# Kernel tuning notes

Hardware: AMD Instinct MI355X
Metric: run time of the kernel (lower is better)

The kernel has to match this reference:

```python
import jax, jax.numpy as jnp
import numpy as np

N = 50000
E = 600000
H = 128


def setup_inputs() -> dict:
    key = jax.random.key(0)
    ks = jax.random.split(key, 9)
    x = jax.random.normal(ks[0], (N, H), dtype=jnp.float32)
    edge_index = jax.random.randint(ks[1], (2, E), 0, N, dtype=jnp.int64)
    edge_weight = jax.random.uniform(ks[2], (E,), dtype=jnp.float32)
    s = 1.0 / np.sqrt(H)
    Wq = jax.random.normal(ks[3], (H, H), dtype=jnp.float32) * s
    bq = jnp.zeros((H,), dtype=jnp.float32)
    Wk = jax.random.normal(ks[4], (H, H), dtype=jnp.float32) * s
    bk = jnp.zeros((H,), dtype=jnp.float32)
    Wv = jax.random.normal(ks[5], (H, H), dtype=jnp.float32) * s
    bv = jnp.zeros((H,), dtype=jnp.float32)
    return {"x": x, "edge_index": edge_index, "edge_weight": edge_weight,
            "Wq": Wq, "bq": bq, "Wk": Wk, "bk": bk, "Wv": Wv, "bv": bv}


def reference(x, edge_index, edge_weight, Wq, bq, Wk, bk, Wv, bv):
    scale = jnp.sqrt(jnp.asarray(x.shape[-1], dtype=x.dtype))
    Q = x @ Wq.T + bq  # [N, H]
    K = x @ Wk.T + bk
    V = x @ Wv.T + bv
    row, col = edge_index[0], edge_index[1]  # [E]
    # per-edge scaled dot-product
    energy = jnp.sum(Q[row] * K[col], axis=-1) / scale  # [E]
    # NOTE: faithful to the source — softmax over ALL edges (dim=0), not per-node
    attn = jax.nn.softmax(energy * edge_weight, axis=0)  # [E]
    msgs = V[col] * attn[:, None]  # [E, H]
    out = jnp.zeros_like(x).at[row].add(msgs)  # scatter-add to destination nodes
    return out
```

## Files before the change

### kernel.cpp

```cpp
#include <hip/hip_runtime.h>
#include <hip/hip_bf16.h>

#define N_NODES 50000
#define E_EDGES 600000
#define HDIM    128

#define QKV_BLOCKS  ((N_NODES + 63) / 64)
#define EDGE_BLOCKS ((E_EDGES + 255) / 256)
#define SCAN_BLOCKS ((N_NODES + 255) / 256)
#define ROW_BLOCKS  (N_NODES / 4)

typedef float f32x4  __attribute__((ext_vector_type(4)));
typedef short short8 __attribute__((ext_vector_type(8)));

__device__ __forceinline__ unsigned short f2bf(float f) {
    __hip_bfloat16 h = __float2bfloat16(f);
    return *reinterpret_cast<unsigned short*>(&h);
}

__global__ __launch_bounds__(256) void qkv_mfma_kernel(
    const float* __restrict__ x,
    const float* __restrict__ Wq, const float* __restrict__ bq,
    const float* __restrict__ Wk, const float* __restrict__ bk,
    const float* __restrict__ Wv, const float* __restrict__ bv,
    float* __restrict__ Q, unsigned short* __restrict__ Kb,
    unsigned short* __restrict__ Vb)
{
    __shared__ __align__(16) unsigned short Ah[64 * HDIM];
    __shared__ __align__(16) unsigned short Al[64 * HDIM];
    const int r0  = blockIdx.x * 64;
    const int mat = blockIdx.y;

    for (int t = threadIdx.x; t < 2048; t += 256) {
        const int r  = t >> 5;
        const int k4 = t & 31;
        int gr = r0 + r; if (gr >= N_NODES) gr = N_NODES - 1;
        const float4 xv = *(const float4*)&x[(size_t)gr * HDIM + k4 * 4];
        const unsigned ux = __float_as_uint(xv.x), uy = __float_as_uint(xv.y);
        const unsigned uz = __float_as_uint(xv.z), uw = __float_as_uint(xv.w);
        ushort4 hv, lv;
        hv.x = (unsigned short)(ux >> 16); hv.y = (unsigned short)(uy >> 16);
        hv.z = (unsigned short)(uz >> 16); hv.w = (unsigned short)(uw >> 16);
        lv.x = f2bf(xv.x - __uint_as_float(ux & 0xffff0000u));
        lv.y = f2bf(xv.y - __uint_as_float(uy & 0xffff0000u));
        lv.z = f2bf(xv.z - __uint_as_float(uz & 0xffff0000u));
        lv.w = f2bf(xv.w - __uint_as_float(uw & 0xffff0000u));
        const int byte = (r << 8) + (k4 << 3);
        const int swz  = byte ^ ((r & 7) << 4);
        *(ushort4*)((char*)Ah + swz) = hv;
        *(ushort4*)((char*)Al + swz) = lv;
    }

    const int lane = threadIdx.x & 63;
    const int w    = threadIdx.x >> 6;
    const int lrow = lane & 15;
    const int lgrp = lane >> 4;
    const int nb   = w * 32;

    const float* Wm = (mat == 0) ? Wq : (mat == 1) ? Wk : Wv;
    const float* bm = (mat == 0) ? bq : (mat == 1) ? bk : bv;

    short8 Bh[2][4], Bl[2][4];
#pragma unroll
    for (int st = 0; st < 2; ++st) {
        const int col = nb + st * 16 + lrow;
#pragma unroll
        for (int ks = 0; ks < 4; ++ks) {
            const int k0 = ks * 32 + lgrp * 8;
            const float* p = Wm + (size_t)col * HDIM + k0;
            const float4 a = *(const float4*)p;
            const float4 b = *(const float4*)(p + 4);
            const float f[8] = {a.x, a.y, a.z, a.w, b.x, b.y, b.z, b.w};
            short8 h, l;
#pragma unroll
            for (int j = 0; j < 8; ++j) {
                const unsigned u = __float_as_uint(f[j]);
                h[j] = (short)(u >> 16);
                l[j] = (short)f2bf(f[j] - __uint_as_float(u & 0xffff0000u));
            }
            Bh[st][ks] = h; Bl[st][ks] = l;
        }
    }
    const float bias0 = bm[nb + lrow];
    const float bias1 = bm[nb + 16 + lrow];

    __syncthreads();

#pragma unroll
    for (int s = 0; s < 4; ++s) {
        f32x4 acc0 = {0.f, 0.f, 0.f, 0.f};
        f32x4 acc1 = {0.f, 0.f, 0.f, 0.f};
        const int row = s * 16 + lrow;
#pragma unroll
        for (int ks = 0; ks < 4; ++ks) {
            const int byte = (row << 8) + ((ks * 32 + lgrp * 8) << 1);
            const int swz  = byte ^ ((row & 7) << 4);
            const short8 ah = *(const short8*)((const char*)Ah + swz);
            const short8 al = *(const short8*)((const char*)Al + swz);
            acc0 = __builtin_amdgcn_mfma_f32_16x16x32_bf16(ah, Bh[0][ks], acc0, 0, 0, 0);
            acc0 = __builtin_amdgcn_mfma_f32_16x16x32_bf16(al, Bh[0][ks], acc0, 0, 0, 0);
            acc0 = __builtin_amdgcn_mfma_f32_16x16x32_bf16(ah, Bl[0][ks], acc0, 0, 0, 0);
            acc1 = __builtin_amdgcn_mfma_f32_16x16x32_bf16(ah, Bh[1][ks], acc1, 0, 0, 0);
            acc1 = __builtin_amdgcn_mfma_f32_16x16x32_bf16(al, Bh[1][ks], acc1, 0, 0, 0);
            acc1 = __builtin_amdgcn_mfma_f32_16x16x32_bf16(ah, Bl[1][ks], acc1, 0, 0, 0);
        }
        const int orow0 = r0 + s * 16 + lgrp * 4;
        if (mat == 0) {
#pragma unroll
            for (int i = 0; i < 4; ++i) {
                const int row_o = orow0 + i;
                if (row_o < N_NODES) {
                    Q[(size_t)row_o * HDIM + nb + lrow]      = acc0[i] + bias0;
                    Q[(size_t)row_o * HDIM + nb + 16 + lrow] = acc1[i] + bias1;
                }
            }
        } else {
            unsigned short* dst = (mat == 1) ? Kb : Vb;
#pragma unroll
            for (int i = 0; i < 4; ++i) {
                const int row_o = orow0 + i;
                if (row_o < N_NODES) {
                    dst[(size_t)row_o * HDIM + nb + lrow]      = f2bf(acc0[i] + bias0);
                    dst[(size_t)row_o * HDIM + nb + 16 + lrow] = f2bf(acc1[i] + bias1);
                }
            }
        }
    }
}

__global__ __launch_bounds__(256) void hist_kernel(
    const int* __restrict__ ei, int* __restrict__ counts)
{
    const int e = blockIdx.x * 256 + threadIdx.x;
    if (e < E_EDGES) atomicAdd(&counts[ei[e]], 1);
}

__global__ __launch_bounds__(256) void scan_partial_kernel(
    const int* __restrict__ counts, int* __restrict__ offs, int* __restrict__ aux)
{
    __shared__ int s[256];
    const int i = blockIdx.x * 256 + threadIdx.x;
    const int v = (i < N_NODES) ? counts[i] : 0;
    s[threadIdx.x] = v;
    __syncthreads();
    for (int d = 1; d < 256; d <<= 1) {
        int t = (threadIdx.x >= d) ? s[threadIdx.x - d] : 0;
        __syncthreads();
        s[threadIdx.x] += t;
        __syncthreads();
    }
    if (i < N_NODES) offs[i] = s[threadIdx.x] - v;
    if (threadIdx.x == 255) aux[blockIdx.x] = s[255];
}

__global__ __launch_bounds__(256) void scan_aux_kernel(int* __restrict__ aux)
{
    __shared__ int s[256];
    const int i = threadIdx.x;
    const int v = (i < SCAN_BLOCKS) ? aux[i] : 0;
    s[i] = v;
    __syncthreads();
    for (int d = 1; d < 256; d <<= 1) {
        int t = (i >= d) ? s[i - d] : 0;
        __syncthreads();
        s[i] += t;
        __syncthreads();
    }
    if (i < SCAN_BLOCKS) aux[i] = s[i] - v;
}

__global__ __launch_bounds__(256) void scan_add_kernel(
    int* __restrict__ offs, const int* __restrict__ aux, int* __restrict__ cursor)
{
    const int i = blockIdx.x * 256 + threadIdx.x;
    if (i < N_NODES) {
        const int o = offs[i] + aux[blockIdx.x];
        offs[i] = o;
        cursor[i] = o;
    }
}

__global__ __launch_bounds__(256) void bin_kernel(
    const int* __restrict__ ei, const float* __restrict__ ew,
    int* __restrict__ cursor, uint2* __restrict__ erec)
{
    const int e = blockIdx.x * 256 + threadIdx.x;
    if (e >= E_EDGES) return;
    const int row = ei[e];
    const int pos = atomicAdd(&cursor[row], 1);
    erec[pos] = make_uint2((unsigned)ei[E_EDGES + e], __float_as_uint(ew[e]));
}

__global__ __launch_bounds__(256) void energy_kernel(
    const float* __restrict__ Q, const unsigned short* __restrict__ Kb,
    const int* __restrict__ offs, const int* __restrict__ counts,
    uint2* __restrict__ erec, float* __restrict__ blockmax)
{
    const int row  = (blockIdx.x * 256 + threadIdx.x) >> 6;
    const int lane = threadIdx.x & 63;
    const int eg   = lane >> 4;
    const int sl   = lane & 15;
    const int start = offs[row], len = counts[row];
    const float4 q0 = *(const float4*)&Q[(size_t)row * HDIM + sl * 8];
    const float4 q1 = *(const float4*)&Q[(size_t)row * HDIM + sl * 8 + 4];
    const uint4* kb128 = (const uint4*)Kb;
    const float inv_scale = 0.08838834764831845f;
    float lmax = -3.4e38f;
    for (int j0 = 0; j0 < len; j0 += 8) {
        const int  jA = j0 + eg,      jB = j0 + 4 + eg;
        const bool vA = jA < len,     vB = jB < len;
        const int  eA = start + (vA ? jA : 0);
        const int  eB = start + (vB ? jB : 0);
        const uint2 rA = erec[eA];
        const uint2 rB = erec[eB];
        const uint4 uA = kb128[(size_t)rA.x * 16 + sl];
        const uint4 uB = kb128[(size_t)rB.x * 16 + sl];
        float dA = q0.x * __uint_as_float(uA.x << 16)
                 + q0.y * __uint_as_float(uA.x & 0xffff0000u)
                 + q0.z * __uint_as_float(uA.y << 16)
                 + q0.w * __uint_as_float(uA.y & 0xffff0000u)
                 + q1.x * __uint_as_float(uA.z << 16)
                 + q1.y * __uint_as_float(uA.z & 0xffff0000u)
                 + q1.z * __uint_as_float(uA.w << 16)
                 + q1.w * __uint_as_float(uA.w & 0xffff0000u);
        float dB = q0.x * __uint_as_float(uB.x << 16)
                 + q0.y * __uint_as_float(uB.x & 0xffff0000u)
                 + q0.z * __uint_as_float(uB.y << 16)
                 + q0.w * __uint_as_float(uB.y & 0xffff0000u)
                 + q1.x * __uint_as_float(uB.z << 16)
                 + q1.y * __uint_as_float(uB.z & 0xffff0000u)
                 + q1.z * __uint_as_float(uB.w << 16)
                 + q1.w * __uint_as_float(uB.w & 0xffff0000u);
#pragma unroll
        for (int m = 8; m >= 1; m >>= 1) {
            dA += __shfl_xor(dA, m);
            dB += __shfl_xor(dB, m);
        }
        const float enA = dA * inv_scale * __uint_as_float(rA.y);
        const float enB = dB * inv_scale * __uint_as_float(rB.y);
        if (vA) {
            lmax = fmaxf(lmax, enA);
            if (sl == 0) ((float*)erec)[2 * eA + 1] = enA;
        }
        if (vB) {
            lmax = fmaxf(lmax, enB);
            if (sl == 0) ((float*)erec)[2 * eB + 1] = enB;
        }
    }
#pragma unroll
    for (int m = 32; m >= 1; m >>= 1) lmax = fmaxf(lmax, __shfl_xor(lmax, m));
    __shared__ float sm[4];
    if (lane == 0) sm[threadIdx.x >> 6] = lmax;
    __syncthreads();
    if (threadIdx.x == 0)
        blockmax[blockIdx.x] = fmaxf(fmaxf(sm[0], sm[1]), fmaxf(sm[2], sm[3]));
}

__global__ __launch_bounds__(256) void reduce_max_kernel(
    const float* __restrict__ bm, int n, float* __restrict__ gmax)
{
    float m = -3.4e38f;
    for (int i = threadIdx.x; i < n; i += 256) m = fmaxf(m, bm[i]);
#pragma unroll
    for (int s = 32; s >= 1; s >>= 1) m = fmaxf(m, __shfl_xor(m, s));
    __shared__ float sm[4];
    if ((threadIdx.x & 63) == 0) sm[threadIdx.x >> 6] = m;
    __syncthreads();
    if (threadIdx.x == 0) *gmax = fmaxf(fmaxf(sm[0], sm[1]), fmaxf(sm[2], sm[3]));
}

__global__ __launch_bounds__(256) void expsum_kernel(
    uint2* __restrict__ erec, const float* __restrict__ gmax,
    float* __restrict__ blocksum)
{
    const float m = *gmax;
    const int e = blockIdx.x * 256 + threadIdx.x;
    float p = 0.f;
    if (e < E_EDGES) {
        const uint2 r = erec[e];
        p = __expf(__uint_as_float(r.y) - m);
        erec[e] = make_uint2(r.x, __float_as_uint(p));
    }
#pragma unroll
    for (int s = 32; s >= 1; s >>= 1) p += __shfl_xor(p, s);
    __shared__ float sm[4];
    if ((threadIdx.x & 63) == 0) sm[threadIdx.x >> 6] = p;
    __syncthreads();
    if (threadIdx.x == 0) blocksum[blockIdx.x] = sm[0] + sm[1] + sm[2] + sm[3];
}

__global__ __launch_bounds__(256) void reduce_sum_kernel(
    const float* __restrict__ bs, int n, float* __restrict__ gsum)
{
    float v = 0.f;
    for (int i = threadIdx.x; i < n; i += 256) v += bs[i];
#pragma unroll
    for (int s = 32; s >= 1; s >>= 1) v += __shfl_xor(v, s);
    __shared__ float sm[4];
    if ((threadIdx.x & 63) == 0) sm[threadIdx.x >> 6] = v;
    __syncthreads();
    if (threadIdx.x == 0) *gsum = sm[0] + sm[1] + sm[2] + sm[3];
}

__global__ __launch_bounds__(256) void accum_kernel(
    const unsigned short* __restrict__ Vb,
    const int* __restrict__ offs, const int* __restrict__ counts,
    const uint2* __restrict__ erec, const float* __restrict__ gsum,
    float* __restrict__ out)
{
    const int row  = (blockIdx.x * 256 + threadIdx.x) >> 6;
    const int lane = threadIdx.x & 63;
    const int eg   = lane >> 4;
    const int sl   = lane & 15;
    const float inv = 1.0f / *gsum;
    const int start = offs[row], len = counts[row];
    const uint4* vb128 = (const uint4*)Vb;
    float aA[8] = {0.f, 0.f, 0.f, 0.f, 0.f, 0.f, 0.f, 0.f};
    float aB[8] = {0.f, 0.f, 0.f, 0.f, 0.f, 0.f, 0.f, 0.f};
    for (int j0 = 0; j0 < len; j0 += 8) {
        const int  jA = j0 + eg,      jB = j0 + 4 + eg;
        const bool vA = jA < len,     vB = jB < len;
        const int  eA = start + (vA ? jA : 0);
        const int  eB = start + (vB ? jB : 0);
        const uint2 rA = erec[eA];
        const uint2 rB = erec[eB];
        const float wA = vA ? __uint_as_float(rA.y) * inv : 0.f;
        const float wB = vB ? __uint_as_float(rB.y) * inv : 0.f;
        const uint4 uA = vb128[(size_t)rA.x * 16 + sl];
        const uint4 uB = vb128[(size_t)rB.x * 16 + sl];
        aA[0] += __uint_as_float(uA.x << 16) * wA;
        aA[1] += __uint_as_float(uA.x & 0xffff0000u) * wA;
        aA[2] += __uint_as_float(uA.y << 16) * wA;
        aA[3] += __uint_as_float(uA.y & 0xffff0000u) * wA;
        aA[4] += __uint_as_float(uA.z << 16) * wA;
        aA[5] += __uint_as_float(uA.z & 0xffff0000u) * wA;
        aA[6] += __uint_as_float(uA.w << 16) * wA;
        aA[7] += __uint_as_float(uA.w & 0xffff0000u) * wA;
        aB[0] += __uint_as_float(uB.x << 16) * wB;
        aB[1] += __uint_as_float(uB.x & 0xffff0000u) * wB;
        aB[2] += __uint_as_float(uB.y << 16) * wB;
        aB[3] += __uint_as_float(uB.y & 0xffff0000u) * wB;
        aB[4] += __uint_as_float(uB.z << 16) * wB;
        aB[5] += __uint_as_float(uB.z & 0xffff0000u) * wB;
        aB[6] += __uint_as_float(uB.w << 16) * wB;
        aB[7] += __uint_as_float(uB.w & 0xffff0000u) * wB;
    }
    float a[8];
#pragma unroll
    for (int i = 0; i < 8; ++i) {
        a[i] = aA[i] + aB[i];
        a[i] += __shfl_xor(a[i], 16);
        a[i] += __shfl_xor(a[i], 32);
    }
    if (eg == 0) {
        float* o = out + (size_t)row * HDIM + sl * 8;
        *(float4*)o       = make_float4(a[0], a[1], a[2], a[3]);
        *(float4*)(o + 4) = make_float4(a[4], a[5], a[6], a[7]);
    }
}

extern "C" void kernel_launch(void* const* d_in, const int* in_sizes, int n_in,
                              void* d_out, int out_size, void* d_ws, size_t ws_size,
                              hipStream_t stream)
{
    const float* x  = (const float*)d_in[0];
    const int*   ei = (const int*)d_in[1];
    const float* ew = (const float*)d_in[2];
    const float* Wq = (const float*)d_in[3];
    const float* bq = (const float*)d_in[4];
    const float* Wk = (const float*)d_in[5];
    const float* bk = (const float*)d_in[6];
    const float* Wv = (const float*)d_in[7];
    const float* bv = (const float*)d_in[8];
    float* out = (float*)d_out;

    float* ws = (float*)d_ws;
    float* Q       = ws;
    unsigned short* Kb = (unsigned short*)(Q + (size_t)N_NODES * HDIM);
    unsigned short* Vb = Kb + (size_t)N_NODES * HDIM;
    int*   counts  = (int*)(Vb + (size_t)N_NODES * HDIM);
    int*   offs    = counts + N_NODES;
    int*   cursor  = offs + N_NODES;
    int*   aux     = cursor + N_NODES;
    uint2* erec    = (uint2*)(aux + 256);
    float* blockmax= (float*)(erec + E_EDGES);
    float* blocksum= blockmax + ROW_BLOCKS;
    float* gmax    = blocksum + EDGE_BLOCKS;
    float* gsum    = gmax + 1;

    hipMemsetAsync(counts, 0, N_NODES * sizeof(int), stream);

    qkv_mfma_kernel<<<dim3(QKV_BLOCKS, 3), 256, 0, stream>>>(
        x, Wq, bq, Wk, bk, Wv, bv, Q, Kb, Vb);
    hist_kernel<<<EDGE_BLOCKS, 256, 0, stream>>>(ei, counts);
    scan_partial_kernel<<<SCAN_BLOCKS, 256, 0, stream>>>(counts, offs, aux);
    scan_aux_kernel<<<1, 256, 0, stream>>>(aux);
    scan_add_kernel<<<SCAN_BLOCKS, 256, 0, stream>>>(offs, aux, cursor);
    bin_kernel<<<EDGE_BLOCKS, 256, 0, stream>>>(ei, ew, cursor, erec);
    energy_kernel<<<ROW_BLOCKS, 256, 0, stream>>>(Q, Kb, offs, counts, erec, blockmax);
    reduce_max_kernel<<<1, 256, 0, stream>>>(blockmax, ROW_BLOCKS, gmax);
    expsum_kernel<<<EDGE_BLOCKS, 256, 0, stream>>>(erec, gmax, blocksum);
    reduce_sum_kernel<<<1, 256, 0, stream>>>(blocksum, EDGE_BLOCKS, gsum);
    accum_kernel<<<ROW_BLOCKS, 256, 0, stream>>>(Vb, offs, counts, erec, gsum, out);
}
```

Before: 188.5 us.

## Replace single-block reductions with global atomics and merge QKV projections per block

Removes the two single-block reduce kernels for the softmax max and sum. They are replaced by an atomicMax on an order-preserving unsigned encoding of the float, and by a float atomicAdd issued from each block. The QKV projection kernel now loops over the three weight matrices inside one block, so the x tile staged in shared memory is reused instead of being reloaded by three separate blocks. This trades kernel launches and x reloads for atomic contention and lower grid parallelism in the QKV kernel, and float atomicAdd makes the sum order nondeterministic.

```diff
diff --git a/kernel.cpp b/kernel.cpp
--- a/kernel.cpp
+++ b/kernel.cpp
@@ -16,6 +16,15 @@
 __device__ __forceinline__ unsigned short f2bf(float f) {
     __hip_bfloat16 h = __float2bfloat16(f);
     return *reinterpret_cast<unsigned short*>(&h);
+}
+
+__device__ __forceinline__ unsigned fenc(float f) {
+    unsigned u = __float_as_uint(f);
+    return (u & 0x80000000u) ? ~u : (u | 0x80000000u);
+}
+__device__ __forceinline__ float fdec(unsigned v) {
+    unsigned u = (v & 0x80000000u) ? (v ^ 0x80000000u) : ~v;
+    return __uint_as_float(u);
 }
 
 __global__ __launch_bounds__(256) void qkv_mfma_kernel(
@@ -28,8 +37,7 @@
 {
     __shared__ __align__(16) unsigned short Ah[64 * HDIM];
     __shared__ __align__(16) unsigned short Al[64 * HDIM];
-    const int r0  = blockIdx.x * 64;
-    const int mat = blockIdx.y;
+    const int r0 = blockIdx.x * 64;
 
     for (int t = threadIdx.x; t < 2048; t += 256) {
         const int r  = t >> 5;
@@ -50,6 +58,7 @@
         *(ushort4*)((char*)Ah + swz) = hv;
         *(ushort4*)((char*)Al + swz) = lv;
     }
+    __syncthreads();
 
     const int lane = threadIdx.x & 63;
     const int w    = threadIdx.x >> 6;
@@ -57,71 +66,71 @@
     const int lgrp = lane >> 4;
     const int nb   = w * 32;
 
-    const float* Wm = (mat == 0) ? Wq : (mat == 1) ? Wk : Wv;
-    const float* bm = (mat == 0) ? bq : (mat == 1) ? bk : bv;
-
-    short8 Bh[2][4], Bl[2][4];
-#pragma unroll
-    for (int st = 0; st < 2; ++st) {
-        const int col = nb + st * 16 + lrow;
-#pragma unroll
-        for (int ks = 0; ks < 4; ++ks) {
-            const int k0 = ks * 32 + lgrp * 8;
-            const float* p = Wm + (size_t)col * HDIM + k0;
-            const float4 a = *(const float4*)p;
-            const float4 b = *(const float4*)(p + 4);
-            const float f[8] = {a.x, a.y, a.z, a.w, b.x, b.y, b.z, b.w};
-            short8 h, l;
-#pragma unroll
-            for (int j = 0; j < 8; ++j) {
-                const unsigned u = __float_as_uint(f[j]);
-                h[j] = (short)(u >> 16);
-                l[j] = (short)f2bf(f[j] - __uint_as_float(u & 0xffff0000u));
+    for (int mat = 0; mat < 3; ++mat) {
+        const float* Wm = (mat == 0) ? Wq : (mat == 1) ? Wk : Wv;
+        const float* bm = (mat == 0) ? bq : (mat == 1) ? bk : bv;
+
+        short8 Bh[2][4], Bl[2][4];
+#pragma unroll
+        for (int st = 0; st < 2; ++st) {
+            const int col = nb + st * 16 + lrow;
+#pragma unroll
+            for (int ks = 0; ks < 4; ++ks) {
+                const int k0 = ks * 32 + lgrp * 8;
+                const float* p = Wm + (size_t)col * HDIM + k0;
+                const float4 a = *(const float4*)p;
+                const float4 b = *(const float4*)(p + 4);
+                const float f[8] = {a.x, a.y, a.z, a.w, b.x, b.y, b.z, b.w};
+                short8 h, l;
+#pragma unroll
+                for (int j = 0; j < 8; ++j) {
+                    const unsigned u = __float_as_uint(f[j]);
+                    h[j] = (short)(u >> 16);
+                    l[j] = (short)f2bf(f[j] - __uint_as_float(u & 0xffff0000u));
+                }
+                Bh[st][ks] = h; Bl[st][ks] = l;
             }
-            Bh[st][ks] = h; Bl[st][ks] = l;
-        }
-    }
-    const float bias0 = bm[nb + lrow];
-    const float bias1 = bm[nb + 16 + lrow];
-
-    __syncthreads();
-
-#pragma unroll
-    for (int s = 0; s < 4; ++s) {
-        f32x4 acc0 = {0.f, 0.f, 0.f, 0.f};
-        f32x4 acc1 = {0.f, 0.f, 0.f, 0.f};
-        const int row = s * 16 + lrow;
-#pragma unroll
-        for (int ks = 0; ks < 4; ++ks) {
-            const int byte = (row << 8) + ((ks * 32 + lgrp * 8) << 1);
-            const int swz  = byte ^ ((row & 7) << 4);
-            const short8 ah = *(const short8*)((const char*)Ah + swz);
-            const short8 al = *(const short8*)((const char*)Al + swz);
-            acc0 = __builtin_amdgcn_mfma_f32_16x16x32_bf16(ah, Bh[0][ks], acc0, 0, 0, 0);
-            acc0 = __builtin_amdgcn_mfma_f32_16x16x32_bf16(al, Bh[0][ks], acc0, 0, 0, 0);
-            acc0 = __builtin_amdgcn_mfma_f32_16x16x32_bf16(ah, Bl[0][ks], acc0, 0, 0, 0);
-            acc1 = __builtin_amdgcn_mfma_f32_16x16x32_bf16(ah, Bh[1][ks], acc1, 0, 0, 0);
-            acc1 = __builtin_amdgcn_mfma_f32_16x16x32_bf16(al, Bh[1][ks], acc1, 0, 0, 0);
-            acc1 = __builtin_amdgcn_mfma_f32_16x16x32_bf16(ah, Bl[1][ks], acc1, 0, 0, 0);
-        }
-        const int orow0 = r0 + s * 16 + lgrp * 4;
-        if (mat == 0) {
-#pragma unroll
-            for (int i = 0; i < 4; ++i) {
-                const int row_o = orow0 + i;
-                if (row_o < N_NODES) {
-                    Q[(size_t)row_o * HDIM + nb + lrow]      = acc0[i] + bias0;
-                    Q[(size_t)row_o * HDIM + nb + 16 + lrow] = acc1[i] + bias1;
+        }
+        const float bias0 = bm[nb + lrow];
+        const float bias1 = bm[nb + 16 + lrow];
+
+#pragma unroll
+        for (int s = 0; s < 4; ++s) {
+            f32x4 acc0 = {0.f, 0.f, 0.f, 0.f};
+            f32x4 acc1 = {0.f, 0.f, 0.f, 0.f};
+            const int row = s * 16 + lrow;
+#pragma unroll
+            for (int ks = 0; ks < 4; ++ks) {
+                const int byte = (row << 8) + ((ks * 32 + lgrp * 8) << 1);
+                const int swz  = byte ^ ((row & 7) << 4);
+                const short8 ah = *(const short8*)((const char*)Ah + swz);
+                const short8 al = *(const short8*)((const char*)Al + swz);
+                acc0 = __builtin_amdgcn_mfma_f32_16x16x32_bf16(ah, Bh[0][ks], acc0, 0, 0, 0);
+                acc0 = __builtin_amdgcn_mfma_f32_16x16x32_bf16(al, Bh[0][ks], acc0, 0, 0, 0);
+                acc0 = __builtin_amdgcn_mfma_f32_16x16x32_bf16(ah, Bl[0][ks], acc0, 0, 0, 0);
+                acc1 = __builtin_amdgcn_mfma_f32_16x16x32_bf16(ah, Bh[1][ks], acc1, 0, 0, 0);
+                acc1 = __builtin_amdgcn_mfma_f32_16x16x32_bf16(al, Bh[1][ks], acc1, 0, 0, 0);
+                acc1 = __builtin_amdgcn_mfma_f32_16x16x32_bf16(ah, Bl[1][ks], acc1, 0, 0, 0);
+            }
+            const int orow0 = r0 + s * 16 + lgrp * 4;
+            if (mat == 0) {
+#pragma unroll
+                for (int i = 0; i < 4; ++i) {
+                    const int row_o = orow0 + i;
+                    if (row_o < N_NODES) {
+                        Q[(size_t)row_o * HDIM + nb + lrow]      = acc0[i] + bias0;
+                        Q[(size_t)row_o * HDIM + nb + 16 + lrow] = acc1[i] + bias1;
+                    }
                 }
-            }
-        } else {
-            unsigned short* dst = (mat == 1) ? Kb : Vb;
-#pragma unroll
-            for (int i = 0; i < 4; ++i) {
-                const int row_o = orow0 + i;
-                if (row_o < N_NODES) {
-                    dst[(size_t)row_o * HDIM + nb + lrow]      = f2bf(acc0[i] + bias0);
-                    dst[(size_t)row_o * HDIM + nb + 16 + lrow] = f2bf(acc1[i] + bias1);
+            } else {
+                unsigned short* dst = (mat == 1) ? Kb : Vb;
+#pragma unroll
+                for (int i = 0; i < 4; ++i) {
+                    const int row_o = orow0 + i;
+                    if (row_o < N_NODES) {
+                        dst[(size_t)row_o * HDIM + nb + lrow]      = f2bf(acc0[i] + bias0);
+                        dst[(size_t)row_o * HDIM + nb + 16 + lrow] = f2bf(acc1[i] + bias1);
+                    }
                 }
             }
         }
@@ -194,7 +203,7 @@
 __global__ __launch_bounds__(256) void energy_kernel(
     const float* __restrict__ Q, const unsigned short* __restrict__ Kb,
     const int* __restrict__ offs, const int* __restrict__ counts,
-    uint2* __restrict__ erec, float* __restrict__ blockmax)
+    uint2* __restrict__ erec, unsigned* __restrict__ gmax_enc)
 {
     const int row  = (blockIdx.x * 256 + threadIdx.x) >> 6;
     const int lane = threadIdx.x & 63;
@@ -253,27 +262,14 @@
     if (lane == 0) sm[threadIdx.x >> 6] = lmax;
     __syncthreads();
     if (threadIdx.x == 0)
-        blockmax[blockIdx.x] = fmaxf(fmaxf(sm[0], sm[1]), fmaxf(sm[2], sm[3]));
-}
-
-__global__ __launch_bounds__(256) void reduce_max_kernel(
-    const float* __restrict__ bm, int n, float* __restrict__ gmax)
-{
-    float m = -3.4e38f;
-    for (int i = threadIdx.x; i < n; i += 256) m = fmaxf(m, bm[i]);
-#pragma unroll
-    for (int s = 32; s >= 1; s >>= 1) m = fmaxf(m, __shfl_xor(m, s));
-    __shared__ float sm[4];
-    if ((threadIdx.x & 63) == 0) sm[threadIdx.x >> 6] = m;
-    __syncthreads();
-    if (threadIdx.x == 0) *gmax = fmaxf(fmaxf(sm[0], sm[1]), fmaxf(sm[2], sm[3]));
+        atomicMax(gmax_enc, fenc(fmaxf(fmaxf(sm[0], sm[1]), fmaxf(sm[2], sm[3]))));
 }
 
 __global__ __launch_bounds__(256) void expsum_kernel(
-    uint2* __restrict__ erec, const float* __restrict__ gmax,
-    float* __restrict__ blocksum)
-{
-    const float m = *gmax;
+    uint2* __restrict__ erec, const unsigned* __restrict__ gmax_enc,
+    float* __restrict__ gsum)
+{
+    const float m = fdec(*gmax_enc);
     const int e = blockIdx.x * 256 + threadIdx.x;
     float p = 0.f;
     if (e < E_EDGES) {
@@ -286,20 +282,7 @@
     __shared__ float sm[4];
     if ((threadIdx.x & 63) == 0) sm[threadIdx.x >> 6] = p;
     __syncthreads();
-    if (threadIdx.x == 0) blocksum[blockIdx.x] = sm[0] + sm[1] + sm[2] + sm[3];
-}
-
-__global__ __launch_bounds__(256) void reduce_sum_kernel(
-    const float* __restrict__ bs, int n, float* __restrict__ gsum)
-{
-    float v = 0.f;
-    for (int i = threadIdx.x; i < n; i += 256) v += bs[i];
-#pragma unroll
-    for (int s = 32; s >= 1; s >>= 1) v += __shfl_xor(v, s);
-    __shared__ float sm[4];
-    if ((threadIdx.x & 63) == 0) sm[threadIdx.x >> 6] = v;
-    __syncthreads();
-    if (threadIdx.x == 0) *gsum = sm[0] + sm[1] + sm[2] + sm[3];
+    if (threadIdx.x == 0) atomicAdd(gsum, sm[0] + sm[1] + sm[2] + sm[3]);
 }
 
 __global__ __launch_bounds__(256) void accum_kernel(
@@ -378,28 +361,24 @@
     float* Q       = ws;
     unsigned short* Kb = (unsigned short*)(Q + (size_t)N_NODES * HDIM);
     unsigned short* Vb = Kb + (size_t)N_NODES * HDIM;
-    int*   counts  = (int*)(Vb + (size_t)N_NODES * HDIM);
+    unsigned* gmax_enc = (unsigned*)(Vb + (size_t)N_NODES * HDIM);
+    float*    gsum     = (float*)(gmax_enc + 1);
+    int*   counts  = (int*)(gsum + 1);
     int*   offs    = counts + N_NODES;
     int*   cursor  = offs + N_NODES;
     int*   aux     = cursor + N_NODES;
     uint2* erec    = (uint2*)(aux + 256);
-    float* blockmax= (float*)(erec + E_EDGES);
-    float* blocksum= blockmax + ROW_BLOCKS;
-    float* gmax    = blocksum + EDGE_BLOCKS;
-    float* gsum    = gmax + 1;
-
-    hipMemsetAsync(counts, 0, N_NODES * sizeof(int), stream);
-
-    qkv_mfma_kernel<<<dim3(QKV_BLOCKS, 3), 256, 0, stream>>>(
+
+    hipMemsetAsync(gmax_enc, 0, (2 + N_NODES) * sizeof(int), stream);
+
+    qkv_mfma_kernel<<<QKV_BLOCKS, 256, 0, stream>>>(
         x, Wq, bq, Wk, bk, Wv, bv, Q, Kb, Vb);
     hist_kernel<<<EDGE_BLOCKS, 256, 0, stream>>>(ei, counts);
     scan_partial_kernel<<<SCAN_BLOCKS, 256, 0, stream>>>(counts, offs, aux);
     scan_aux_kernel<<<1, 256, 0, stream>>>(aux);
     scan_add_kernel<<<SCAN_BLOCKS, 256, 0, stream>>>(offs, aux, cursor);
     bin_kernel<<<EDGE_BLOCKS, 256, 0, stream>>>(ei, ew, cursor, erec);
-    energy_kernel<<<ROW_BLOCKS, 256, 0, stream>>>(Q, Kb, offs, counts, erec, blockmax);
-    reduce_max_kernel<<<1, 256, 0, stream>>>(blockmax, ROW_BLOCKS, gmax);
-    expsum_kernel<<<EDGE_BLOCKS, 256, 0, stream>>>(erec, gmax, blocksum);
-    reduce_sum_kernel<<<1, 256, 0, stream>>>(blocksum, EDGE_BLOCKS, gsum);
+    energy_kernel<<<ROW_BLOCKS, 256, 0, stream>>>(Q, Kb, offs, counts, erec, gmax_enc);
+    expsum_kernel<<<EDGE_BLOCKS, 256, 0, stream>>>(erec, gmax_enc, gsum);
     accum_kernel<<<ROW_BLOCKS, 256, 0, stream>>>(Vb, offs, counts, erec, gsum, out);
 }
```

Measured after the change: 360.0 us. +91.0%, slower.
